# Kernel tuning notes

Measured on AMD Instinct MI355X. Metric: run time of the kernel, lower is better.

## Reference

```python
import jax, jax.numpy as jnp
import numpy as np

NUM_STUDENTS = 50000
NUM_KP = 100
KD = 128          # knowledge_dim
HID = 256         # hidden_dim
B = 16384
K = 20            # max_knowledge_points


def setup_inputs() -> dict:
    key = jax.random.key(0)
    ks = jax.random.split(key, 16)
    inp = {
        "student_indices": jax.random.randint(ks[0], (B,), 0, NUM_STUDENTS, dtype=jnp.int32),
        "kp_indices": jax.random.randint(ks[1], (B, K), 0, NUM_KP, dtype=jnp.int32),
        "kp_lengths": jax.random.randint(ks[2], (B,), 0, K + 1, dtype=jnp.int32),
        # learned parameters
        "emb": jax.random.normal(ks[3], (NUM_STUDENTS, NUM_KP, KD), dtype=jnp.float32),
        # attention: Linear(KD,HID) -> tanh -> Linear(HID,1) -> softmax(dim=1)
        "W1": jax.random.normal(ks[4], (KD, HID), dtype=jnp.float32) * 0.05,
        "b1": jnp.zeros((HID,), jnp.float32),
        "w2": jax.random.normal(ks[5], (HID, 1), dtype=jnp.float32) * 0.05,
        "b2": jnp.zeros((1,), jnp.float32),
        # MLP: Linear(KD,HID)-ReLU-Linear(HID,HID//2)-ReLU-Linear(HID//2,1)-Sigmoid
        "M1": jax.random.normal(ks[6], (KD, HID), dtype=jnp.float32) * 0.05,
        "mb1": jnp.zeros((HID,), jnp.float32),
        "M2": jax.random.normal(ks[7], (HID, HID // 2), dtype=jnp.float32) * 0.05,
        "mb2": jnp.zeros((HID // 2,), jnp.float32),
        "M3": jax.random.normal(ks[8], (HID // 2, 1), dtype=jnp.float32) * 0.05,
        "mb3": jnp.zeros((1,), jnp.float32),
    }
    return inp


def reference(student_indices, kp_indices, kp_lengths, emb, W1, b1, w2, b2,
              M1, mb1, M2, mb2, M3, mb3):
    # ragged gather -> padded [B, K, KD]; padded slots are zero (as in the torch loop)
    vecs = emb[student_indices[:, None], kp_indices]            # [B,K,KD]
    mask = (jnp.arange(K)[None, :] < kp_lengths[:, None]).astype(vecs.dtype)  # [B,K]
    vecs = vecs * mask[:, :, None]
    # attention: Linear-Tanh-Linear-Softmax(dim=1), THEN masked (matches original order)
    logits = jnp.tanh(vecs @ W1 + b1) @ w2 + b2                 # [B,K,1]
    att = jax.nn.softmax(logits, axis=1) * mask[:, :, None]     # [B,K,1]
    weighted = jnp.sum(att * vecs, axis=1)                      # [B,KD]
    # MLP (dropout = identity in eval)
    h = jax.nn.relu(weighted @ M1 + mb1)
    h = jax.nn.relu(h @ M2 + mb2)
    scores = jax.nn.sigmoid(h @ M3 + mb3)[:, 0]                 # [B]
    return scores, att[:, :, 0]
```

## Files before the change

### kernel.cpp

```cpp
#include <hip/hip_runtime.h>
#include <hip/hip_bf16.h>

#define K_ 20
#define KD_ 128
#define HID_ 256
#define NKP_ 100

using short8_t = __attribute__((ext_vector_type(8))) short;
using f32x4 = __attribute__((ext_vector_type(4))) float;

__device__ __forceinline__ unsigned short f2bf(float f) {
    union { __hip_bfloat16 h; unsigned short u; } c; c.h = __float2bfloat16(f); return c.u;
}
__device__ __forceinline__ float vexp(float x) { float r; asm("v_exp_f32 %0, %1" : "=v"(r) : "v"(x)); return r; }
__device__ __forceinline__ float vrcp(float x) { float r; asm("v_rcp_f32 %0, %1" : "=v"(r) : "v"(x)); return r; }

#define CEXP 2.885390081777927f

__global__ __launch_bounds__(256) void prep_frags(
    const float* __restrict__ W1, const float* __restrict__ M1,
    const float* __restrict__ M2, unsigned short* __restrict__ w1f,
    unsigned short* __restrict__ m1f, unsigned short* __restrict__ m2f)
{
    const int b = blockIdx.x;
    const float* src; unsigned short* dst; int nc, smask, nshift, ib;
    if (b < 128)      { src = W1; dst = w1f; nc = 256; smask = 3; nshift = 2; ib = b; }
    else if (b < 256) { src = M1; dst = m1f; nc = 256; smask = 3; nshift = 2; ib = b - 128; }
    else              { src = M2; dst = m2f; nc = 128; smask = 7; nshift = 3; ib = b - 256; }
    const int i = ib * 256 + threadIdx.x;
    const int j = i & 7, l = (i >> 3) & 63, f = i >> 9;
    const int s = f & smask, n = f >> nshift;
    const int k = s * 32 + (l >> 4) * 8 + j;
    const int col = n * 16 + (l & 15);
    dst[i] = f2bf(src[k * nc + col]);
}

__global__ __launch_bounds__(256, 3) void cdm_attn(
    const int* __restrict__ stu_idx, const int* __restrict__ kp_idx,
    const int* __restrict__ kp_len, const float* __restrict__ emb,
    const unsigned short* __restrict__ w1f,
    const float* __restrict__ b1, const float* __restrict__ w2,
    const float* __restrict__ b2,
    float* __restrict__ out_att, unsigned short* __restrict__ wsum_g)
{
    const int tid = threadIdx.x, lane = tid & 63, w = tid >> 6;
    const int base = blockIdx.x * 8;

    __shared__ unsigned short vec_s[8][K_][KD_];
    __shared__ float lp_s[2][2][4][24];
    __shared__ float l0_s[4];

    short8_t Bf[4][4];
    {
        const short8_t* bfr = (const short8_t*)w1f;
#pragma unroll
        for (int nn = 0; nn < 4; ++nn)
#pragma unroll
            for (int s = 0; s < 4; ++s)
                Bf[nn][s] = bfr[((w * 4 + nn) * 4 + s) * 64 + lane];
    }

    float b1C[4], w2r[4], n2r[4];
#pragma unroll
    for (int nn = 0; nn < 4; ++nn) {
        const int c = (w * 4 + nn) * 16 + (lane & 15);
        b1C[nn] = b1[c] * CEXP;
        w2r[nn] = w2[c];
        n2r[nn] = -2.f * w2r[nn];
    }
    const float b2v = b2[0];

    for (int h = 0; h < 2; ++h) {
        const int gs = base + 2 * w + h;
        const int len = kp_len[gs];
        const long long eb = (long long)stu_idx[gs] * (NKP_ * KD_);
        const int g = lane >> 4, c16 = lane & 15;
        float4 va[5], vb[5];
#pragma unroll
        for (int it = 0; it < 5; ++it) {
            va[it] = make_float4(0.f, 0.f, 0.f, 0.f);
            vb[it] = make_float4(0.f, 0.f, 0.f, 0.f);
            const int r = it * 4 + g;
            if (r < len) {
                const int kp = kp_idx[gs * K_ + r];
                const float4* src = (const float4*)(emb + eb + (long long)kp * KD_) + c16 * 2;
                va[it] = src[0]; vb[it] = src[1];
            }
        }
        char* sb = (char*)&vec_s[2 * w + h][0][0];
#pragma unroll
        for (int it = 0; it < 5; ++it) {
            const int r = it * 4 + g;
            short8_t pk;
            pk[0] = (short)f2bf(va[it].x); pk[1] = (short)f2bf(va[it].y);
            pk[2] = (short)f2bf(va[it].z); pk[3] = (short)f2bf(va[it].w);
            pk[4] = (short)f2bf(vb[it].x); pk[5] = (short)f2bf(vb[it].y);
            pk[6] = (short)f2bf(vb[it].z); pk[7] = (short)f2bf(vb[it].w);
            *(short8_t*)(sb + r * 256 + ((c16 * 16) ^ ((r & 7) << 4))) = pk;
        }
    }

    {
        float p = 0.f;
#pragma unroll
        for (int nn = 0; nn < 4; ++nn)
            p = fmaf(n2r[nn], vrcp(vexp(b1C[nn]) + 1.f), p + w2r[nn]);
#pragma unroll
        for (int m = 1; m <= 8; m <<= 1) p += __shfl_xor(p, m);
        if (lane == 0) l0_s[w] = p;
    }
    __syncthreads();
    const float logit0 = l0_s[0] + l0_s[1] + l0_s[2] + l0_s[3] + b2v;

    for (int p = 0; p < 4; ++p) {
        const int sp = 2 * p;
        const int lA = kp_len[base + sp], lB = kp_len[base + sp + 1];
        const bool need2 = (lA > 16) || (lB > 16);

        short8_t A0[4], A1[4];
        {
            const char* bA = (const char*)&vec_s[sp][0][0];
            const char* bB = (const char*)&vec_s[sp + 1][0][0];
            const int lr = lane & 15;
            const int rowb = lr * 256;
#pragma unroll
            for (int s = 0; s < 4; ++s) {
                const int colA = (s * 64 + (lane >> 4) * 16) ^ ((lr & 7) << 4);
                A0[s] = *(const short8_t*)(bA + rowb + colA);
                A1[s] = *(const short8_t*)(bB + rowb + colA);
            }
        }

        float lp0[4] = {0, 0, 0, 0}, lp1[4] = {0, 0, 0, 0};
#pragma unroll
        for (int nn = 0; nn < 4; ++nn) {
            f32x4 a0 = {0.f, 0.f, 0.f, 0.f}, a1 = {0.f, 0.f, 0.f, 0.f};
#pragma unroll
            for (int s = 0; s < 4; ++s) {
                a0 = __builtin_amdgcn_mfma_f32_16x16x32_bf16(A0[s], Bf[nn][s], a0, 0, 0, 0);
                a1 = __builtin_amdgcn_mfma_f32_16x16x32_bf16(A1[s], Bf[nn][s], a1, 0, 0, 0);
            }
            const float bc = b1C[nn], wv = w2r[nn], n2 = n2r[nn];
#pragma unroll
            for (int i = 0; i < 4; ++i) {
                lp0[i] = fmaf(n2, vrcp(vexp(fmaf(a0[i], CEXP, bc)) + 1.f), lp0[i] + wv);
                lp1[i] = fmaf(n2, vrcp(vexp(fmaf(a1[i], CEXP, bc)) + 1.f), lp1[i] + wv);
            }
        }
#pragma unroll
        for (int i = 0; i < 4; ++i) {
#pragma unroll
            for (int m = 1; m <= 8; m <<= 1) {
                lp0[i] += __shfl_xor(lp0[i], m);
                lp1[i] += __shfl_xor(lp1[i], m);
            }
        }
        const int par = p & 1;
        if ((lane & 15) == 0) {
            const int g = lane >> 4;
#pragma unroll
            for (int i = 0; i < 4; ++i) {
                lp_s[par][0][w][g * 4 + i] = lp0[i];
                lp_s[par][1][w][g * 4 + i] = lp1[i];
            }
        }

        if (need2) {
            short8_t A2[4];
            const int lr = lane & 15;
            const char* t2b = (const char*)&vec_s[sp + ((lr >> 2) & 1)][0][0] + (16 + (lr & 3)) * 256;
            const bool v2 = lr < 8;
            const short8_t z = {0, 0, 0, 0, 0, 0, 0, 0};
#pragma unroll
            for (int s = 0; s < 4; ++s) {
                const int colT = s * 64 + (lane >> 4) * 16;
                const short8_t t = *(const short8_t*)(t2b + (colT ^ ((lr & 3) << 4)));
                A2[s] = v2 ? t : z;
            }
            float lp2[4] = {0, 0, 0, 0};
#pragma unroll
            for (int nn = 0; nn < 4; ++nn) {
                f32x4 a2 = {0.f, 0.f, 0.f, 0.f};
#pragma unroll
                for (int s = 0; s < 4; ++s)
                    a2 = __builtin_amdgcn_mfma_f32_16x16x32_bf16(A2[s], Bf[nn][s], a2, 0, 0, 0);
                const float bc = b1C[nn], wv = w2r[nn], n2 = n2r[nn];
#pragma unroll
                for (int i = 0; i < 4; ++i)
                    lp2[i] = fmaf(n2, vrcp(vexp(fmaf(a2[i], CEXP, bc)) + 1.f), lp2[i] + wv);
            }
#pragma unroll
            for (int i = 0; i < 4; ++i) {
#pragma unroll
                for (int m = 1; m <= 8; m <<= 1) lp2[i] += __shfl_xor(lp2[i], m);
            }
            if ((lane & 15) == 0 && (lane >> 4) < 2) {
                const int g = lane >> 4;
#pragma unroll
                for (int i = 0; i < 4; ++i) lp_s[par][g][w][16 + i] = lp2[i];
            }
        }
        __syncthreads();

        const int j = lane & 31, hh = lane >> 5;
        const int gsS = base + sp + hh;
        const int lenS = hh ? lB : lA;
        float logit = -1e30f;
        if (j < K_) {
            logit = (j < lenS)
                ? b2v + lp_s[par][hh][0][j] + lp_s[par][hh][1][j]
                      + lp_s[par][hh][2][j] + lp_s[par][hh][3][j]
                : logit0;
        }
        float mx = logit;
#pragma unroll
        for (int m = 16; m >= 1; m >>= 1) mx = fmaxf(mx, __shfl_xor(mx, m, 32));
        const float e = (j < K_) ? vexp((logit - mx) * 1.44269504f) : 0.f;
        float sm = e;
#pragma unroll
        for (int m = 16; m >= 1; m >>= 1) sm += __shfl_xor(sm, m, 32);
        const float attv = (j < lenS) ? e * vrcp(sm) : 0.f;
        if (w == 0 && j < K_) out_att[gsS * K_ + j] = attv;

        const int d = w * 32 + (lane & 31);
        const char* vb2 = (const char*)&vec_s[sp + hh][0][0];
        const int lm = max(lA, lB);
        float sacc = 0.f;
        for (int k = 0; k < lm; ++k) {
            const unsigned short u = *(const unsigned short*)(vb2 + k * 256 + ((2 * d) ^ ((k & 7) << 4)));
            const float av = __shfl(attv, k + (lane & 32));
            sacc = fmaf(av, __uint_as_float(((unsigned)u) << 16), sacc);
        }
        wsum_g[gsS * KD_ + d] = f2bf(sacc);
    }
}

__global__ __launch_bounds__(256, 3) void cdm_mlp(
    const unsigned short* __restrict__ wsum_g,
    const unsigned short* __restrict__ m1f, const unsigned short* __restrict__ m2f,
    const float* __restrict__ mb1, const float* __restrict__ mb2,
    const float* __restrict__ M3, const float* __restrict__ mb3,
    float* __restrict__ out_scores)
{
    const int tid = threadIdx.x, lane = tid & 63, w = tid >> 6;
    const int S0 = blockIdx.x * 32;

    __shared__ unsigned short h1_s[32][HID_];
    __shared__ float sc_s[4][32];

    short8_t Aw[2][4];
#pragma unroll
    for (int m = 0; m < 2; ++m)
#pragma unroll
        for (int s = 0; s < 4; ++s)
            Aw[m][s] = *(const short8_t*)(wsum_g + (S0 + m * 16 + (lane & 15)) * KD_
                                          + s * 32 + (lane >> 4) * 8);
    short8_t B1r[4][4];
    {
        const short8_t* bf1 = (const short8_t*)m1f;
#pragma unroll
        for (int nn = 0; nn < 4; ++nn)
#pragma unroll
            for (int s = 0; s < 4; ++s)
                B1r[nn][s] = bf1[((w * 4 + nn) * 4 + s) * 64 + lane];
    }
#pragma unroll
    for (int nn = 0; nn < 4; ++nn) {
        f32x4 c0 = {0.f, 0.f, 0.f, 0.f}, c1 = {0.f, 0.f, 0.f, 0.f};
#pragma unroll
        for (int s = 0; s < 4; ++s) {
            c0 = __builtin_amdgcn_mfma_f32_16x16x32_bf16(Aw[0][s], B1r[nn][s], c0, 0, 0, 0);
            c1 = __builtin_amdgcn_mfma_f32_16x16x32_bf16(Aw[1][s], B1r[nn][s], c1, 0, 0, 0);
        }
        const int col = (w * 4 + nn) * 16 + (lane & 15);
        const float bias = mb1[col];
#pragma unroll
        for (int i = 0; i < 4; ++i) {
            const int r0 = (lane >> 4) * 4 + i;
            const int r1 = 16 + r0;
            *(unsigned short*)((char*)h1_s + r0 * 512 + ((2 * col) ^ ((r0 & 7) << 4)))
                = f2bf(fmaxf(c0[i] + bias, 0.f));
            *(unsigned short*)((char*)h1_s + r1 * 512 + ((2 * col) ^ ((r0 & 7) << 4)))
                = f2bf(fmaxf(c1[i] + bias, 0.f));
        }
    }
    __syncthreads();

    short8_t B2r[2][8];
    {
        const short8_t* bf2 = (const short8_t*)m2f;
#pragma unroll
        for (int nn = 0; nn < 2; ++nn)
#pragma unroll
            for (int s = 0; s < 8; ++s)
                B2r[nn][s] = bf2[((w * 2 + nn) * 8 + s) * 64 + lane];
    }
    f32x4 d00 = {0.f, 0.f, 0.f, 0.f}, d01 = {0.f, 0.f, 0.f, 0.f};
    f32x4 d10 = {0.f, 0.f, 0.f, 0.f}, d11 = {0.f, 0.f, 0.f, 0.f};
    {
        const int lr = lane & 15;
#pragma unroll
        for (int s = 0; s < 8; ++s) {
            const int off = (s * 64 + (lane >> 4) * 16) ^ ((lr & 7) << 4);
            const short8_t Ah0 = *(const short8_t*)((const char*)h1_s + lr * 512 + off);
            const short8_t Ah1 = *(const short8_t*)((const char*)h1_s + (16 + lr) * 512 + off);
            d00 = __builtin_amdgcn_mfma_f32_16x16x32_bf16(Ah0, B2r[0][s], d00, 0, 0, 0);
            d01 = __builtin_amdgcn_mfma_f32_16x16x32_bf16(Ah0, B2r[1][s], d01, 0, 0, 0);
            d10 = __builtin_amdgcn_mfma_f32_16x16x32_bf16(Ah1, B2r[0][s], d10, 0, 0, 0);
            d11 = __builtin_amdgcn_mfma_f32_16x16x32_bf16(Ah1, B2r[1][s], d11, 0, 0, 0);
        }
    }
    float part0[4] = {0, 0, 0, 0}, part1[4] = {0, 0, 0, 0};
#pragma unroll
    for (int nn = 0; nn < 2; ++nn) {
        const int col = (w * 2 + nn) * 16 + (lane & 15);
        const float bb = mb2[col], m3v = M3[col];
        const f32x4 dm0 = nn ? d01 : d00;
        const f32x4 dm1 = nn ? d11 : d10;
#pragma unroll
        for (int i = 0; i < 4; ++i) {
            part0[i] = fmaf(fmaxf(dm0[i] + bb, 0.f), m3v, part0[i]);
            part1[i] = fmaf(fmaxf(dm1[i] + bb, 0.f), m3v, part1[i]);
        }
    }
#pragma unroll
    for (int i = 0; i < 4; ++i) {
#pragma unroll
        for (int m = 1; m <= 8; m <<= 1) {
            part0[i] += __shfl_xor(part0[i], m);
            part1[i] += __shfl_xor(part1[i], m);
        }
    }
    if ((lane & 15) == 0) {
        const int g = lane >> 4;
#pragma unroll
        for (int i = 0; i < 4; ++i) {
            sc_s[w][g * 4 + i] = part0[i];
            sc_s[w][16 + g * 4 + i] = part1[i];
        }
    }
    __syncthreads();
    if (tid < 32) {
        const float sc = sc_s[0][tid] + sc_s[1][tid] + sc_s[2][tid] + sc_s[3][tid] + mb3[0];
        out_scores[S0 + tid] = 1.f / (1.f + __expf(-sc));
    }
}

extern "C" void kernel_launch(void* const* d_in, const int* in_sizes, int n_in,
                              void* d_out, int out_size, void* d_ws, size_t ws_size,
                              hipStream_t stream) {
    const int*   stu = (const int*)d_in[0];
    const int*   kpi = (const int*)d_in[1];
    const int*   kpl = (const int*)d_in[2];
    const float* emb = (const float*)d_in[3];
    const float* W1  = (const float*)d_in[4];
    const float* b1  = (const float*)d_in[5];
    const float* w2  = (const float*)d_in[6];
    const float* b2  = (const float*)d_in[7];
    const float* M1  = (const float*)d_in[8];
    const float* mb1 = (const float*)d_in[9];
    const float* M2  = (const float*)d_in[10];
    const float* mb2 = (const float*)d_in[11];
    const float* M3  = (const float*)d_in[12];
    const float* mb3 = (const float*)d_in[13];
    const int B = in_sizes[0];

    float* out_scores = (float*)d_out;
    float* out_att    = out_scores + B;

    unsigned short* w1f  = (unsigned short*)d_ws;
    unsigned short* m1f  = w1f + 32768;
    unsigned short* m2f  = m1f + 32768;
    unsigned short* wsum = m2f + 32768;

    prep_frags<<<384, 256, 0, stream>>>(W1, M1, M2, w1f, m1f, m2f);
    cdm_attn<<<B / 8, 256, 0, stream>>>(stu, kpi, kpl, emb, w1f, b1, w2, b2,
                                        out_att, wsum);
    cdm_mlp<<<B / 32, 256, 0, stream>>>(wsum, m1f, m2f, mb1, mb2, M3, mb3, out_scores);
}
```

Baseline: 88.95 us.

## Fuse attention and MLP kernels into one, keeping weighted sums in LDS

Merges the attention kernel and the MLP kernel into a single kernel. Each block's 8 weighted-sum rows stay in shared memory and run through the two MLP GEMMs with half-empty 16-row MFMA tiles, so the bf16 round trip through global memory and one launch are gone. It also issues all gather loads for both students before any conversion, and caches lengths in LDS. The cost is wasted MFMA work on zero-padded rows, extra LDS and register pressure, and reloading the MLP weight fragments in every one of the smaller blocks.

```diff
diff --git a/kernel.cpp b/kernel.cpp
--- a/kernel.cpp
+++ b/kernel.cpp
@@ -35,13 +35,16 @@
     dst[i] = f2bf(src[k * nc + col]);
 }
 
-__global__ __launch_bounds__(256, 3) void cdm_attn(
+__global__ __launch_bounds__(256, 3) void cdm_fused(
     const int* __restrict__ stu_idx, const int* __restrict__ kp_idx,
     const int* __restrict__ kp_len, const float* __restrict__ emb,
     const unsigned short* __restrict__ w1f,
+    const unsigned short* __restrict__ m1f, const unsigned short* __restrict__ m2f,
     const float* __restrict__ b1, const float* __restrict__ w2,
     const float* __restrict__ b2,
-    float* __restrict__ out_att, unsigned short* __restrict__ wsum_g)
+    const float* __restrict__ mb1, const float* __restrict__ mb2,
+    const float* __restrict__ M3, const float* __restrict__ mb3,
+    float* __restrict__ out_scores, float* __restrict__ out_att)
 {
     const int tid = threadIdx.x, lane = tid & 63, w = tid >> 6;
     const int base = blockIdx.x * 8;
@@ -49,6 +52,50 @@
     __shared__ unsigned short vec_s[8][K_][KD_];
     __shared__ float lp_s[2][2][4][24];
     __shared__ float l0_s[4];
+    __shared__ int   len_s[8];
+    __shared__ unsigned short wsum_s[8][136];
+    __shared__ unsigned short h1_s[8][264];
+    __shared__ float sc_s[4][8];
+
+    {
+        const int g = lane >> 4, c16 = lane & 15;
+        float4 va[10], vb[10];
+        int lens[2];
+#pragma unroll
+        for (int h = 0; h < 2; ++h) {
+            const int gs = base + 2 * w + h;
+            lens[h] = kp_len[gs];
+            const long long eb = (long long)stu_idx[gs] * (NKP_ * KD_);
+#pragma unroll
+            for (int it = 0; it < 5; ++it) {
+                const int q = h * 5 + it;
+                va[q] = make_float4(0.f, 0.f, 0.f, 0.f);
+                vb[q] = make_float4(0.f, 0.f, 0.f, 0.f);
+                const int r = it * 4 + g;
+                if (r < lens[h]) {
+                    const int kp = kp_idx[gs * K_ + r];
+                    const float4* src = (const float4*)(emb + eb + (long long)kp * KD_) + c16 * 2;
+                    va[q] = src[0]; vb[q] = src[1];
+                }
+            }
+        }
+#pragma unroll
+        for (int h = 0; h < 2; ++h) {
+            char* sb = (char*)&vec_s[2 * w + h][0][0];
+#pragma unroll
+            for (int it = 0; it < 5; ++it) {
+                const int q = h * 5 + it;
+                const int r = it * 4 + g;
+                short8_t pk;
+                pk[0] = (short)f2bf(va[q].x); pk[1] = (short)f2bf(va[q].y);
+                pk[2] = (short)f2bf(va[q].z); pk[3] = (short)f2bf(va[q].w);
+                pk[4] = (short)f2bf(vb[q].x); pk[5] = (short)f2bf(vb[q].y);
+                pk[6] = (short)f2bf(vb[q].z); pk[7] = (short)f2bf(vb[q].w);
+                *(short8_t*)(sb + r * 256 + ((c16 * 16) ^ ((r & 7) << 4))) = pk;
+            }
+        }
+        if (lane == 0) { len_s[2 * w] = lens[0]; len_s[2 * w + 1] = lens[1]; }
+    }
 
     short8_t Bf[4][4];
     {
@@ -59,7 +106,6 @@
             for (int s = 0; s < 4; ++s)
                 Bf[nn][s] = bfr[((w * 4 + nn) * 4 + s) * 64 + lane];
     }
-
     float b1C[4], w2r[4], n2r[4];
 #pragma unroll
     for (int nn = 0; nn < 4; ++nn) {
@@ -70,36 +116,6 @@
     }
     const float b2v = b2[0];
 
-    for (int h = 0; h < 2; ++h) {
-        const int gs = base + 2 * w + h;
-        const int len = kp_len[gs];
-        const long long eb = (long long)stu_idx[gs] * (NKP_ * KD_);
-        const int g = lane >> 4, c16 = lane & 15;
-        float4 va[5], vb[5];
-#pragma unroll
-        for (int it = 0; it < 5; ++it) {
-            va[it] = make_float4(0.f, 0.f, 0.f, 0.f);
-            vb[it] = make_float4(0.f, 0.f, 0.f, 0.f);
-            const int r = it * 4 + g;
-            if (r < len) {
-                const int kp = kp_idx[gs * K_ + r];
-                const float4* src = (const float4*)(emb + eb + (long long)kp * KD_) + c16 * 2;
-                va[it] = src[0]; vb[it] = src[1];
-            }
-        }
-        char* sb = (char*)&vec_s[2 * w + h][0][0];
-#pragma unroll
-        for (int it = 0; it < 5; ++it) {
-            const int r = it * 4 + g;
-            short8_t pk;
-            pk[0] = (short)f2bf(va[it].x); pk[1] = (short)f2bf(va[it].y);
-            pk[2] = (short)f2bf(va[it].z); pk[3] = (short)f2bf(va[it].w);
-            pk[4] = (short)f2bf(vb[it].x); pk[5] = (short)f2bf(vb[it].y);
-            pk[6] = (short)f2bf(vb[it].z); pk[7] = (short)f2bf(vb[it].w);
-            *(short8_t*)(sb + r * 256 + ((c16 * 16) ^ ((r & 7) << 4))) = pk;
-        }
-    }
-
     {
         float p = 0.f;
 #pragma unroll
@@ -114,7 +130,7 @@
 
     for (int p = 0; p < 4; ++p) {
         const int sp = 2 * p;
-        const int lA = kp_len[base + sp], lB = kp_len[base + sp + 1];
+        const int lA = len_s[sp], lB = len_s[sp + 1];
         const bool need2 = (lA > 16) || (lB > 16);
 
         short8_t A0[4], A1[4];
@@ -231,30 +247,9 @@
             const float av = __shfl(attv, k + (lane & 32));
             sacc = fmaf(av, __uint_as_float(((unsigned)u) << 16), sacc);
         }
-        wsum_g[gsS * KD_ + d] = f2bf(sacc);
-    }
-}
-
-__global__ __launch_bounds__(256, 3) void cdm_mlp(
-    const unsigned short* __restrict__ wsum_g,
-    const unsigned short* __restrict__ m1f, const unsigned short* __restrict__ m2f,
-    const float* __restrict__ mb1, const float* __restrict__ mb2,
-    const float* __restrict__ M3, const float* __restrict__ mb3,
-    float* __restrict__ out_scores)
-{
-    const int tid = threadIdx.x, lane = tid & 63, w = tid >> 6;
-    const int S0 = blockIdx.x * 32;
-
-    __shared__ unsigned short h1_s[32][HID_];
-    __shared__ float sc_s[4][32];
-
-    short8_t Aw[2][4];
-#pragma unroll
-    for (int m = 0; m < 2; ++m)
-#pragma unroll
-        for (int s = 0; s < 4; ++s)
-            Aw[m][s] = *(const short8_t*)(wsum_g + (S0 + m * 16 + (lane & 15)) * KD_
-                                          + s * 32 + (lane >> 4) * 8);
+        wsum_s[sp + hh][d] = f2bf(sacc);
+    }
+
     short8_t B1r[4][4];
     {
         const short8_t* bf1 = (const short8_t*)m1f;
@@ -264,27 +259,33 @@
             for (int s = 0; s < 4; ++s)
                 B1r[nn][s] = bf1[((w * 4 + nn) * 4 + s) * 64 + lane];
     }
-#pragma unroll
-    for (int nn = 0; nn < 4; ++nn) {
-        f32x4 c0 = {0.f, 0.f, 0.f, 0.f}, c1 = {0.f, 0.f, 0.f, 0.f};
+    __syncthreads();
+
+    {
+        short8_t Aw[4];
+        const int r = lane & 15, g = lane >> 4;
+        const short8_t z8 = {0, 0, 0, 0, 0, 0, 0, 0};
 #pragma unroll
         for (int s = 0; s < 4; ++s) {
-            c0 = __builtin_amdgcn_mfma_f32_16x16x32_bf16(Aw[0][s], B1r[nn][s], c0, 0, 0, 0);
-            c1 = __builtin_amdgcn_mfma_f32_16x16x32_bf16(Aw[1][s], B1r[nn][s], c1, 0, 0, 0);
-        }
-        const int col = (w * 4 + nn) * 16 + (lane & 15);
-        const float bias = mb1[col];
-#pragma unroll
-        for (int i = 0; i < 4; ++i) {
-            const int r0 = (lane >> 4) * 4 + i;
-            const int r1 = 16 + r0;
-            *(unsigned short*)((char*)h1_s + r0 * 512 + ((2 * col) ^ ((r0 & 7) << 4)))
-                = f2bf(fmaxf(c0[i] + bias, 0.f));
-            *(unsigned short*)((char*)h1_s + r1 * 512 + ((2 * col) ^ ((r0 & 7) << 4)))
-                = f2bf(fmaxf(c1[i] + bias, 0.f));
-        }
-    }
-    __syncthreads();
+            const short8_t t = *(const short8_t*)((const char*)wsum_s + (r & 7) * 272 + (s * 32 + g * 8) * 2);
+            Aw[s] = (r < 8) ? t : z8;
+        }
+#pragma unroll
+        for (int nn = 0; nn < 4; ++nn) {
+            f32x4 c = {0.f, 0.f, 0.f, 0.f};
+#pragma unroll
+            for (int s = 0; s < 4; ++s)
+                c = __builtin_amdgcn_mfma_f32_16x16x32_bf16(Aw[s], B1r[nn][s], c, 0, 0, 0);
+            const int col = (w * 4 + nn) * 16 + (lane & 15);
+            const float bias = mb1[col];
+            if (g < 2) {
+#pragma unroll
+                for (int i = 0; i < 4; ++i)
+                    *(unsigned short*)((char*)h1_s + (g * 4 + i) * 528 + col * 2)
+                        = f2bf(fmaxf(c[i] + bias, 0.f));
+            }
+        }
+    }
 
     short8_t B2r[2][8];
     {
@@ -295,54 +296,44 @@
             for (int s = 0; s < 8; ++s)
                 B2r[nn][s] = bf2[((w * 2 + nn) * 8 + s) * 64 + lane];
     }
-    f32x4 d00 = {0.f, 0.f, 0.f, 0.f}, d01 = {0.f, 0.f, 0.f, 0.f};
-    f32x4 d10 = {0.f, 0.f, 0.f, 0.f}, d11 = {0.f, 0.f, 0.f, 0.f};
-    {
-        const int lr = lane & 15;
+    __syncthreads();
+
+    {
+        short8_t Ah[8];
+        const int r = lane & 15, g = lane >> 4;
+        const short8_t z8 = {0, 0, 0, 0, 0, 0, 0, 0};
 #pragma unroll
         for (int s = 0; s < 8; ++s) {
-            const int off = (s * 64 + (lane >> 4) * 16) ^ ((lr & 7) << 4);
-            const short8_t Ah0 = *(const short8_t*)((const char*)h1_s + lr * 512 + off);
-            const short8_t Ah1 = *(const short8_t*)((const char*)h1_s + (16 + lr) * 512 + off);
-            d00 = __builtin_amdgcn_mfma_f32_16x16x32_bf16(Ah0, B2r[0][s], d00, 0, 0, 0);
-            d01 = __builtin_amdgcn_mfma_f32_16x16x32_bf16(Ah0, B2r[1][s], d01, 0, 0, 0);
-            d10 = __builtin_amdgcn_mfma_f32_16x16x32_bf16(Ah1, B2r[0][s], d10, 0, 0, 0);
-            d11 = __builtin_amdgcn_mfma_f32_16x16x32_bf16(Ah1, B2r[1][s], d11, 0, 0, 0);
-        }
-    }
-    float part0[4] = {0, 0, 0, 0}, part1[4] = {0, 0, 0, 0};
-#pragma unroll
-    for (int nn = 0; nn < 2; ++nn) {
-        const int col = (w * 2 + nn) * 16 + (lane & 15);
-        const float bb = mb2[col], m3v = M3[col];
-        const f32x4 dm0 = nn ? d01 : d00;
-        const f32x4 dm1 = nn ? d11 : d10;
+            const short8_t t = *(const short8_t*)((const char*)h1_s + (r & 7) * 528 + (s * 32 + g * 8) * 2);
+            Ah[s] = (r < 8) ? t : z8;
+        }
+        f32x4 d0 = {0.f, 0.f, 0.f, 0.f}, d1 = {0.f, 0.f, 0.f, 0.f};
+#pragma unroll
+        for (int s = 0; s < 8; ++s) {
+            d0 = __builtin_amdgcn_mfma_f32_16x16x32_bf16(Ah[s], B2r[0][s], d0, 0, 0, 0);
+            d1 = __builtin_amdgcn_mfma_f32_16x16x32_bf16(Ah[s], B2r[1][s], d1, 0, 0, 0);
+        }
+        const int c0 = (w * 2) * 16 + (lane & 15), c1 = c0 + 16;
+        const float mbA = mb2[c0], m3A = M3[c0];
+        const float mbB = mb2[c1], m3B = M3[c1];
+        float part[4];
+#pragma unroll
+        for (int i = 0; i < 4; ++i)
+            part[i] = fmaxf(d0[i] + mbA, 0.f) * m3A + fmaxf(d1[i] + mbB, 0.f) * m3B;
 #pragma unroll
         for (int i = 0; i < 4; ++i) {
-            part0[i] = fmaf(fmaxf(dm0[i] + bb, 0.f), m3v, part0[i]);
-            part1[i] = fmaf(fmaxf(dm1[i] + bb, 0.f), m3v, part1[i]);
-        }
-    }
-#pragma unroll
-    for (int i = 0; i < 4; ++i) {
-#pragma unroll
-        for (int m = 1; m <= 8; m <<= 1) {
-            part0[i] += __shfl_xor(part0[i], m);
-            part1[i] += __shfl_xor(part1[i], m);
-        }
-    }
-    if ((lane & 15) == 0) {
-        const int g = lane >> 4;
-#pragma unroll
-        for (int i = 0; i < 4; ++i) {
-            sc_s[w][g * 4 + i] = part0[i];
-            sc_s[w][16 + g * 4 + i] = part1[i];
+#pragma unroll
+            for (int m = 1; m <= 8; m <<= 1) part[i] += __shfl_xor(part[i], m);
+        }
+        if ((lane & 15) == 0 && g < 2) {
+#pragma unroll
+            for (int i = 0; i < 4; ++i) sc_s[w][g * 4 + i] = part[i];
         }
     }
     __syncthreads();
-    if (tid < 32) {
+    if (tid < 8) {
         const float sc = sc_s[0][tid] + sc_s[1][tid] + sc_s[2][tid] + sc_s[3][tid] + mb3[0];
-        out_scores[S0 + tid] = 1.f / (1.f + __expf(-sc));
+        out_scores[base + tid] = 1.f / (1.f + __expf(-sc));
     }
 }
 
@@ -368,13 +359,12 @@
     float* out_scores = (float*)d_out;
     float* out_att    = out_scores + B;
 
-    unsigned short* w1f  = (unsigned short*)d_ws;
-    unsigned short* m1f  = w1f + 32768;
-    unsigned short* m2f  = m1f + 32768;
-    unsigned short* wsum = m2f + 32768;
+    unsigned short* w1f = (unsigned short*)d_ws;
+    unsigned short* m1f = w1f + 32768;
+    unsigned short* m2f = m1f + 32768;
 
     prep_frags<<<384, 256, 0, stream>>>(W1, M1, M2, w1f, m1f, m2f);
-    cdm_attn<<<B / 8, 256, 0, stream>>>(stu, kpi, kpl, emb, w1f, b1, w2, b2,
-                                        out_att, wsum);
-    cdm_mlp<<<B / 32, 256, 0, stream>>>(wsum, m1f, m2f, mb1, mb2, M3, mb3, out_scores);
+    cdm_fused<<<B / 8, 256, 0, stream>>>(stu, kpi, kpl, emb, w1f, m1f, m2f,
+                                         b1, w2, b2, mb1, mb2, M3, mb3,
+                                         out_scores, out_att);
 }
```

After: 106.0 us. +19.2%, slower.

## Batch gather loads, defer softmax to one sync, vectorize weighted sum

Applied to the files above, without the earlier changes.

The gather now issues the loads for both samples per wave before any bf16 conversion and does this before the W1 fragment loads, so more memory requests are in flight at once. The logit partials for all four sample pairs go to a larger shared buffer. This replaces the per-pair barrier with a single barrier, after which each wave runs softmax and the weighted sum for its own two samples. The weighted sum reads four bf16 values per lane with a uint2 load and writes packed output. The cost is more registers (ten float4 pairs live at once), which may hurt occupancy at the three-blocks-per-SM bound.

```diff
diff --git a/kernel.cpp b/kernel.cpp
--- a/kernel.cpp
+++ b/kernel.cpp
@@ -14,6 +14,8 @@
 }
 __device__ __forceinline__ float vexp(float x) { float r; asm("v_exp_f32 %0, %1" : "=v"(r) : "v"(x)); return r; }
 __device__ __forceinline__ float vrcp(float x) { float r; asm("v_rcp_f32 %0, %1" : "=v"(r) : "v"(x)); return r; }
+__device__ __forceinline__ float bf_lo(unsigned u) { return __uint_as_float(u << 16); }
+__device__ __forceinline__ float bf_hi(unsigned u) { return __uint_as_float(u & 0xffff0000u); }
 
 #define CEXP 2.885390081777927f
 
@@ -47,8 +49,49 @@
     const int base = blockIdx.x * 8;
 
     __shared__ unsigned short vec_s[8][K_][KD_];
-    __shared__ float lp_s[2][2][4][24];
+    __shared__ float lp_s[4][2][4][24];
     __shared__ float l0_s[4];
+    __shared__ int   len_s[8];
+
+    {
+        const int g = lane >> 4, c16 = lane & 15;
+        float4 va[10], vb[10];
+        int lens[2];
+#pragma unroll
+        for (int h = 0; h < 2; ++h) {
+            const int gs = base + 2 * w + h;
+            lens[h] = kp_len[gs];
+            const long long eb = (long long)stu_idx[gs] * (NKP_ * KD_);
+#pragma unroll
+            for (int it = 0; it < 5; ++it) {
+                const int q = h * 5 + it;
+                va[q] = make_float4(0.f, 0.f, 0.f, 0.f);
+                vb[q] = make_float4(0.f, 0.f, 0.f, 0.f);
+                const int r = it * 4 + g;
+                if (r < lens[h]) {
+                    const int kp = kp_idx[gs * K_ + r];
+                    const float4* src = (const float4*)(emb + eb + (long long)kp * KD_) + c16 * 2;
+                    va[q] = src[0]; vb[q] = src[1];
+                }
+            }
+        }
+#pragma unroll
+        for (int h = 0; h < 2; ++h) {
+            char* sb = (char*)&vec_s[2 * w + h][0][0];
+#pragma unroll
+            for (int it = 0; it < 5; ++it) {
+                const int q = h * 5 + it;
+                const int r = it * 4 + g;
+                short8_t pk;
+                pk[0] = (short)f2bf(va[q].x); pk[1] = (short)f2bf(va[q].y);
+                pk[2] = (short)f2bf(va[q].z); pk[3] = (short)f2bf(va[q].w);
+                pk[4] = (short)f2bf(vb[q].x); pk[5] = (short)f2bf(vb[q].y);
+                pk[6] = (short)f2bf(vb[q].z); pk[7] = (short)f2bf(vb[q].w);
+                *(short8_t*)(sb + r * 256 + ((c16 * 16) ^ ((r & 7) << 4))) = pk;
+            }
+        }
+        if (lane == 0) { len_s[2 * w] = lens[0]; len_s[2 * w + 1] = lens[1]; }
+    }
 
     short8_t Bf[4][4];
     {
@@ -59,7 +102,6 @@
             for (int s = 0; s < 4; ++s)
                 Bf[nn][s] = bfr[((w * 4 + nn) * 4 + s) * 64 + lane];
     }
-
     float b1C[4], w2r[4], n2r[4];
 #pragma unroll
     for (int nn = 0; nn < 4; ++nn) {
@@ -70,36 +112,6 @@
     }
     const float b2v = b2[0];
 
-    for (int h = 0; h < 2; ++h) {
-        const int gs = base + 2 * w + h;
-        const int len = kp_len[gs];
-        const long long eb = (long long)stu_idx[gs] * (NKP_ * KD_);
-        const int g = lane >> 4, c16 = lane & 15;
-        float4 va[5], vb[5];
-#pragma unroll
-        for (int it = 0; it < 5; ++it) {
-            va[it] = make_float4(0.f, 0.f, 0.f, 0.f);
-            vb[it] = make_float4(0.f, 0.f, 0.f, 0.f);
-            const int r = it * 4 + g;
-            if (r < len) {
-                const int kp = kp_idx[gs * K_ + r];
-                const float4* src = (const float4*)(emb + eb + (long long)kp * KD_) + c16 * 2;
-                va[it] = src[0]; vb[it] = src[1];
-            }
-        }
-        char* sb = (char*)&vec_s[2 * w + h][0][0];
-#pragma unroll
-        for (int it = 0; it < 5; ++it) {
-            const int r = it * 4 + g;
-            short8_t pk;
-            pk[0] = (short)f2bf(va[it].x); pk[1] = (short)f2bf(va[it].y);
-            pk[2] = (short)f2bf(va[it].z); pk[3] = (short)f2bf(va[it].w);
-            pk[4] = (short)f2bf(vb[it].x); pk[5] = (short)f2bf(vb[it].y);
-            pk[6] = (short)f2bf(vb[it].z); pk[7] = (short)f2bf(vb[it].w);
-            *(short8_t*)(sb + r * 256 + ((c16 * 16) ^ ((r & 7) << 4))) = pk;
-        }
-    }
-
     {
         float p = 0.f;
 #pragma unroll
@@ -112,9 +124,10 @@
     __syncthreads();
     const float logit0 = l0_s[0] + l0_s[1] + l0_s[2] + l0_s[3] + b2v;
 
+#pragma unroll
     for (int p = 0; p < 4; ++p) {
         const int sp = 2 * p;
-        const int lA = kp_len[base + sp], lB = kp_len[base + sp + 1];
+        const int lA = len_s[sp], lB = len_s[sp + 1];
         const bool need2 = (lA > 16) || (lB > 16);
 
         short8_t A0[4], A1[4];
@@ -155,13 +168,12 @@
                 lp1[i] += __shfl_xor(lp1[i], m);
             }
         }
-        const int par = p & 1;
         if ((lane & 15) == 0) {
             const int g = lane >> 4;
 #pragma unroll
             for (int i = 0; i < 4; ++i) {
-                lp_s[par][0][w][g * 4 + i] = lp0[i];
-                lp_s[par][1][w][g * 4 + i] = lp1[i];
+                lp_s[p][0][w][g * 4 + i] = lp0[i];
+                lp_s[p][1][w][g * 4 + i] = lp1[i];
             }
         }
 
@@ -197,19 +209,22 @@
             if ((lane & 15) == 0 && (lane >> 4) < 2) {
                 const int g = lane >> 4;
 #pragma unroll
-                for (int i = 0; i < 4; ++i) lp_s[par][g][w][16 + i] = lp2[i];
-            }
-        }
-        __syncthreads();
-
+                for (int i = 0; i < 4; ++i) lp_s[p][g][w][16 + i] = lp2[i];
+            }
+        }
+    }
+    __syncthreads();
+
+    {
         const int j = lane & 31, hh = lane >> 5;
-        const int gsS = base + sp + hh;
-        const int lenS = hh ? lB : lA;
+        const int smp = 2 * w + hh;
+        const int gsS = base + smp;
+        const int lenS = len_s[smp];
         float logit = -1e30f;
         if (j < K_) {
             logit = (j < lenS)
-                ? b2v + lp_s[par][hh][0][j] + lp_s[par][hh][1][j]
-                      + lp_s[par][hh][2][j] + lp_s[par][hh][3][j]
+                ? b2v + lp_s[w][hh][0][j] + lp_s[w][hh][1][j]
+                      + lp_s[w][hh][2][j] + lp_s[w][hh][3][j]
                 : logit0;
         }
         float mx = logit;
@@ -220,18 +235,24 @@
 #pragma unroll
         for (int m = 16; m >= 1; m >>= 1) sm += __shfl_xor(sm, m, 32);
         const float attv = (j < lenS) ? e * vrcp(sm) : 0.f;
-        if (w == 0 && j < K_) out_att[gsS * K_ + j] = attv;
-
-        const int d = w * 32 + (lane & 31);
-        const char* vb2 = (const char*)&vec_s[sp + hh][0][0];
-        const int lm = max(lA, lB);
-        float sacc = 0.f;
+        if (j < K_) out_att[gsS * K_ + j] = attv;
+
+        const int d0 = (lane & 31) * 4;
+        const char* vb2 = (const char*)&vec_s[smp][0][0];
+        const int lm = max(len_s[2 * w], len_s[2 * w + 1]);
+        float s0 = 0.f, s1 = 0.f, s2 = 0.f, s3 = 0.f;
         for (int k = 0; k < lm; ++k) {
-            const unsigned short u = *(const unsigned short*)(vb2 + k * 256 + ((2 * d) ^ ((k & 7) << 4)));
             const float av = __shfl(attv, k + (lane & 32));
-            sacc = fmaf(av, __uint_as_float(((unsigned)u) << 16), sacc);
-        }
-        wsum_g[gsS * KD_ + d] = f2bf(sacc);
+            const uint2 u = *(const uint2*)(vb2 + k * 256 + ((2 * d0) ^ ((k & 7) << 4)));
+            s0 = fmaf(av, bf_lo(u.x), s0);
+            s1 = fmaf(av, bf_hi(u.x), s1);
+            s2 = fmaf(av, bf_lo(u.y), s2);
+            s3 = fmaf(av, bf_hi(u.y), s3);
+        }
+        uint2 pk;
+        pk.x = (unsigned)f2bf(s0) | ((unsigned)f2bf(s1) << 16);
+        pk.y = (unsigned)f2bf(s2) | ((unsigned)f2bf(s3) << 16);
+        *(uint2*)(wsum_g + gsS * KD_ + d0) = pk;
     }
 }
 
```

Result: faster. 78.08 us (-12.2%).
